# Kernel optimization log

Hardware: AMD Instinct MI355X
Metric: run time of the kernel (lower is better)

## Reference

```python
import jax, jax.numpy as jnp
import numpy as np

DIM = 1024
H = 16
D = DIM // H  # 64
EPS = 1e-6


def _rmsnorm(x, scale):
    # per-last-dim RMSNorm, computed in fp32 like the torch code
    rms = jax.lax.rsqrt(jnp.mean(x * x, axis=-1, keepdims=True) + EPS)
    return x * rms * scale


def _apply_rope(xq, xk, pe):
    # xq, xk: [B,H,L,D]; pe: [1,1,L,D/2,2,2]
    B, h, L, d = xq.shape
    xq_ = xq.reshape(B, h, L, d // 2, 1, 2)
    xk_ = xk.reshape(B, h, L, d // 2, 1, 2)
    xq_out = pe[..., 0] * xq_[..., 0] + pe[..., 1] * xq_[..., 1]  # [B,H,L,D/2,2]
    xk_out = pe[..., 0] * xk_[..., 0] + pe[..., 1] * xk_[..., 1]
    return xq_out.reshape(B, h, L, d), xk_out.reshape(B, h, L, d)


def setup_inputs() -> dict:
    key = jax.random.key(0)
    ks = jax.random.split(key, 6)
    B, L = 2, 2048
    x = jax.random.normal(ks[0], (B, L, DIM), dtype=jnp.float32)
    pe = jax.random.normal(ks[1], (1, 1, L, D // 2, 2, 2), dtype=jnp.float32)
    qkv_w = jax.random.normal(ks[2], (3 * DIM, DIM), dtype=jnp.float32) * (DIM ** -0.5)
    q_scale = jnp.ones((D,), dtype=jnp.float32)
    k_scale = jnp.ones((D,), dtype=jnp.float32)
    proj_w = jax.random.normal(ks[3], (DIM, DIM), dtype=jnp.float32) * (DIM ** -0.5)
    proj_b = jnp.zeros((DIM,), dtype=jnp.float32)
    return {"x": x, "pe": pe, "qkv_w": qkv_w, "q_scale": q_scale,
            "k_scale": k_scale, "proj_w": proj_w, "proj_b": proj_b}


def reference(x, pe, qkv_w, q_scale, k_scale, proj_w, proj_b):
    B, L, _ = x.shape
    x_c = jnp.clip(jnp.nan_to_num(x, nan=0.0, posinf=0.0, neginf=0.0), -10000.0, 10000.0)
    qkv = x_c @ qkv_w.T  # [B,L,3*DIM] (qkv_bias=False)
    qkv = jnp.nan_to_num(qkv, nan=0.0, posinf=0.0, neginf=0.0)
    # 'B L (K H D) -> K B H L D'
    qkv = qkv.reshape(B, L, 3, H, D).transpose(2, 0, 3, 1, 4)
    q, k, v = qkv[0], qkv[1], qkv[2]  # each [B,H,L,D]
    q = _rmsnorm(q, q_scale)
    k = _rmsnorm(k, k_scale)
    q, k = _apply_rope(q, k, pe)
    # scaled dot product attention (no mask)
    scores = jnp.einsum('bhqd,bhkd->bhqk', q, k) * (D ** -0.5)
    attn = jax.nn.softmax(scores, axis=-1)
    out = jnp.einsum('bhqk,bhkd->bhqd', attn, v)
    out = out.transpose(0, 2, 1, 3).reshape(B, L, H * D)  # 'B H L D -> B L (H D)'
    out = jnp.clip(out, -10000.0, 10000.0)
    return out @ proj_w.T + proj_b
```

## Files before the change

kernel.cpp:

```cpp
#include <hip/hip_runtime.h>
#include <hip/hip_bf16.h>

#define DIMC 1024
#define HEADS 16
#define HD 64
#define BATCH 2
#define SEQ 2048

typedef __bf16 bf16;
typedef __bf16 bf16x4 __attribute__((ext_vector_type(4)));
typedef __bf16 bf16x8 __attribute__((ext_vector_type(8)));
typedef float f32x4 __attribute__((ext_vector_type(4)));

typedef const __attribute__((address_space(1))) void* gas_t;
typedef __attribute__((address_space(3))) void* las_t;

__device__ inline f32x4 mfma_bf16(bf16x8 a, bf16x8 b, f32x4 c) {
    return __builtin_amdgcn_mfma_f32_16x16x32_bf16(a, b, c, 0, 0, 0);
}

__device__ inline void st8(bf16* p, bf16x8 v) {
    *(bf16x4*)p       = *(bf16x4*)&v;
    *(bf16x4*)(p + 4) = *((bf16x4*)&v + 1);
}
__device__ inline bf16x8 ld_frag(const bf16* p) {
    bf16x8 r;
    *(bf16x4*)&r       = *(const bf16x4*)p;
    *((bf16x4*)&r + 1) = *(const bf16x4*)(p + 16);
    return r;
}
__device__ inline bf16x8 ld_frag_c(const bf16* tile, int row, int kk, int lg) {
    const char* rp = (const char*)(tile + row * 64);
    const int p = row & 7;
    const int c0 = kk * 4 + (lg >> 1);
    const int ib = (lg & 1) * 8;
    bf16x8 r;
    *(bf16x4*)&r       = *(const bf16x4*)(rp + ((((c0) ^ p) << 4) | ib));
    *((bf16x4*)&r + 1) = *(const bf16x4*)(rp + ((((c0 + 2) ^ p) << 4) | ib));
    return r;
}

__device__ inline void swz_tile(int nx, int& m0, int& n0) {
    int flat = blockIdx.y * nx + blockIdx.x;
    int cpx = (nx * gridDim.y) >> 3;
    int s = (flat & 7) * cpx + (flat >> 3);
    n0 = (s % nx) * 128;
    m0 = (s / nx) * 128;
}

__global__ __launch_bounds__(256) void k_prep_all(const float* __restrict__ x,
                                                  const float* __restrict__ qw,
                                                  const float* __restrict__ pw,
                                                  bf16* __restrict__ xb,
                                                  bf16* __restrict__ wqkv,
                                                  bf16* __restrict__ wproj) {
    int idx = blockIdx.x * 1024 + threadIdx.x;
#pragma unroll
    for (int j = 0; j < 4; ++j, idx += 256) {
        if (idx < 1048576) {
            float4 v = ((const float4*)x)[idx];
            float a[4] = {v.x, v.y, v.z, v.w};
            bf16x4 o;
#pragma unroll
            for (int q = 0; q < 4; ++q) {
                float f = a[q];
                f = __builtin_isfinite(f) ? fminf(fmaxf(f, -10000.f), 10000.f) : 0.f;
                o[q] = (bf16)f;
            }
            ((bf16x4*)xb)[idx] = o;
        } else if (idx < 1835008) {
            int i2 = idx - 1048576;
            float4 v = ((const float4*)qw)[i2];
            bf16x4 o = {(bf16)v.x, (bf16)v.y, (bf16)v.z, (bf16)v.w};
            ((bf16x4*)wqkv)[i2] = o;
        } else {
            int i2 = idx - 1835008;
            float4 v = ((const float4*)pw)[i2];
            bf16x4 o = {(bf16)v.x, (bf16)v.y, (bf16)v.z, (bf16)v.w};
            ((bf16x4*)wproj)[i2] = o;
        }
    }
}

template <bool OUT_BF16, bool BIAS, bool SANITIZE>
__global__ __launch_bounds__(256) void k_gemm_bt(const bf16* __restrict__ A,
                                                 const bf16* __restrict__ Bt,
                                                 void* __restrict__ Cv,
                                                 const float* __restrict__ bias,
                                                 int N, int K) {
    __shared__ alignas(16) bf16 As[128 * 64];
    __shared__ alignas(16) bf16 Bs[128 * 64];
    const int t = threadIdx.x;
    int m0, n0;
    swz_tile(N >> 7, m0, n0);
    const int w = t >> 6, lane = t & 63;
    const int wm = (w >> 1) * 64, wn = (w & 1) * 64;
    const int lr = lane & 15, lg = lane >> 4;
    const int srow = lane >> 3;
    const int scol = ((lane & 7) ^ srow) * 8;

    f32x4 acc[4][4];
#pragma unroll
    for (int i = 0; i < 4; ++i)
#pragma unroll
        for (int j = 0; j < 4; ++j) acc[i][j] = 0.0f;

    for (int k0 = 0; k0 < K; k0 += 64) {
#pragma unroll
        for (int i = 0; i < 4; ++i) {
            int rg = w * 32 + i * 8;
            __builtin_amdgcn_global_load_lds(
                (gas_t)(A + (size_t)(m0 + rg + srow) * K + k0 + scol),
                (las_t)(As + rg * 64), 16, 0, 0);
            __builtin_amdgcn_global_load_lds(
                (gas_t)(Bt + (size_t)(n0 + rg + srow) * K + k0 + scol),
                (las_t)(Bs + rg * 64), 16, 0, 0);
        }
        __syncthreads();
#pragma unroll
        for (int kk = 0; kk < 2; ++kk) {
            bf16x8 af[4], bfr[4];
#pragma unroll
            for (int mi = 0; mi < 4; ++mi)
                af[mi] = ld_frag_c(As, wm + mi * 16 + lr, kk, lg);
#pragma unroll
            for (int ni = 0; ni < 4; ++ni)
                bfr[ni] = ld_frag_c(Bs, wn + ni * 16 + lr, kk, lg);
#pragma unroll
            for (int mi = 0; mi < 4; ++mi)
#pragma unroll
                for (int ni = 0; ni < 4; ++ni)
                    acc[mi][ni] = mfma_bf16(af[mi], bfr[ni], acc[mi][ni]);
        }
        __syncthreads();
    }
#pragma unroll
    for (int mi = 0; mi < 4; ++mi) {
#pragma unroll
        for (int ni = 0; ni < 4; ++ni) {
            int col = n0 + wn + ni * 16 + lr;
            float bval = BIAS ? bias[col] : 0.f;
#pragma unroll
            for (int r = 0; r < 4; ++r) {
                int row = m0 + wm + mi * 16 + lg * 4 + r;
                float v = acc[mi][ni][r];
                if (SANITIZE) v = __builtin_isfinite(v) ? v : 0.f;
                v += bval;
                if (OUT_BF16)
                    ((bf16*)Cv)[(size_t)row * N + col] = (bf16)v;
                else
                    ((float*)Cv)[(size_t)row * N + col] = v;
            }
        }
    }
}

__global__ __launch_bounds__(256) void k_gemm_qkv(const bf16* __restrict__ A,
                                                  const bf16* __restrict__ Bt,
                                                  const float* __restrict__ pe,
                                                  const float* __restrict__ q_scale,
                                                  const float* __restrict__ k_scale,
                                                  bf16* __restrict__ qb,
                                                  bf16* __restrict__ kb,
                                                  bf16* __restrict__ vt) {
    __shared__ alignas(16) bf16 As[128 * 64];
    __shared__ alignas(16) bf16 Bs[128 * 64];
    const int K = DIMC, t = threadIdx.x;
    int m0, n0;
    swz_tile(24, m0, n0);
    const int w = t >> 6, lane = t & 63;
    const int wm = (w >> 1) * 64, wn = (w & 1) * 64;
    const int lr = lane & 15, lg = lane >> 4;
    const int srow = lane >> 3;
    const int scol = ((lane & 7) ^ srow) * 8;

    f32x4 acc[4][4];
#pragma unroll
    for (int i = 0; i < 4; ++i)
#pragma unroll
        for (int j = 0; j < 4; ++j) acc[i][j] = 0.0f;

    for (int k0 = 0; k0 < K; k0 += 64) {
#pragma unroll
        for (int i = 0; i < 4; ++i) {
            int rg = w * 32 + i * 8;
            __builtin_amdgcn_global_load_lds(
                (gas_t)(A + (size_t)(m0 + rg + srow) * K + k0 + scol),
                (las_t)(As + rg * 64), 16, 0, 0);
            __builtin_amdgcn_global_load_lds(
                (gas_t)(Bt + (size_t)(n0 + rg + srow) * K + k0 + scol),
                (las_t)(Bs + rg * 64), 16, 0, 0);
        }
        __syncthreads();
#pragma unroll
        for (int kk = 0; kk < 2; ++kk) {
            bf16x8 af[4], bfr[4];
#pragma unroll
            for (int mi = 0; mi < 4; ++mi)
                af[mi] = ld_frag_c(As, wm + mi * 16 + lr, kk, lg);
#pragma unroll
            for (int ni = 0; ni < 4; ++ni)
                bfr[ni] = ld_frag_c(Bs, wn + ni * 16 + lr, kk, lg);
#pragma unroll
            for (int mi = 0; mi < 4; ++mi)
#pragma unroll
                for (int ni = 0; ni < 4; ++ni)
                    acc[mi][ni] = mfma_bf16(af[mi], bfr[ni], acc[mi][ni]);
        }
        __syncthreads();
    }

    const int g = (n0 + wn) >> 6;
    const int sel = g >> 4;
    const int hh = g & 15;
    const int row0 = m0 + wm;
    const int bb = row0 >> 11;
    const int l0 = row0 & (SEQ - 1);
    const size_t bhh = (size_t)(bb * HEADS + hh);

#pragma unroll
    for (int mi = 0; mi < 4; ++mi)
#pragma unroll
        for (int ni = 0; ni < 4; ++ni)
#pragma unroll
            for (int r = 0; r < 4; ++r) {
                float v = acc[mi][ni][r];
                acc[mi][ni][r] = __builtin_isfinite(v) ? v : 0.f;
            }

    if (sel == 2) {
#pragma unroll
        for (int mi = 0; mi < 4; ++mi)
#pragma unroll
            for (int ni = 0; ni < 4; ++ni) {
                bf16x4 ov;
#pragma unroll
                for (int r = 0; r < 4; ++r) ov[r] = (bf16)acc[mi][ni][r];
                *(bf16x4*)(vt + (bhh * HD + ni * 16 + lr) * SEQ +
                           l0 + mi * 16 + lg * 4) = ov;
            }
    } else {
        const float* sc = sel ? k_scale : q_scale;
        bf16* dst = sel ? kb : qb;
        const float oscale = sel ? 1.0f : 0.125f * 1.44269504088896340736f;
        float scv[4];
#pragma unroll
        for (int ni = 0; ni < 4; ++ni) scv[ni] = sc[ni * 16 + lr];
#pragma unroll
        for (int mi = 0; mi < 4; ++mi) {
#pragma unroll
            for (int r = 0; r < 4; ++r) {
                float ss = 0.f;
#pragma unroll
                for (int ni = 0; ni < 4; ++ni)
                    ss += acc[mi][ni][r] * acc[mi][ni][r];
                ss += __shfl_xor(ss, 1, 64);
                ss += __shfl_xor(ss, 2, 64);
                ss += __shfl_xor(ss, 4, 64);
                ss += __shfl_xor(ss, 8, 64);
                float rms = rsqrtf(ss * (1.f / 64.f) + 1e-6f);
                int l = l0 + mi * 16 + lg * 4 + r;
                const float* peb = pe + (size_t)l * 128 + (lr & 1) * 2;
                bf16* db = dst + (bhh * SEQ + l) * HD + lr;
#pragma unroll
                for (int ni = 0; ni < 4; ++ni) {
                    float e = acc[mi][ni][r] * rms * scv[ni];
                    float p = __shfl_xor(e, 1, 64);
                    float2 pv = *(const float2*)(peb + (ni * 8 + (lr >> 1)) * 4);
                    float ee = (lr & 1) ? p : e;
                    float eo = (lr & 1) ? e : p;
                    db[ni * 16] = (bf16)((pv.x * ee + pv.y * eo) * oscale);
                }
            }
        }
    }
}

__global__ __launch_bounds__(512) void k_attn(const bf16* __restrict__ Q,
                                              const bf16* __restrict__ Kb,
                                              const bf16* __restrict__ Vt,
                                              bf16* __restrict__ O) {
    __shared__ bf16 Ks[2][128][68];
    __shared__ bf16 Vs[2][2][64][68];
    const int bid = blockIdx.x;
    const int s_id = (bid & 7) * 64 + (bid >> 3);
    const int qt = s_id & 15, bh = s_id >> 4;
    const int b = bh >> 4, h = bh & 15;
    const int t = threadIdx.x, w = t >> 6, lane = t & 63;
    const int lr = lane & 15, lg = lane >> 4;
    const size_t baseQK = (size_t)bh * SEQ * HD;
    const size_t baseVt = (size_t)bh * HD * SEQ;

    const bf16* qp = Q + baseQK + (size_t)(qt * 128 + w * 16 + lr) * HD;
    bf16x8 qf0 = ld_frag(qp + lg * 4);
    bf16x8 qf1 = ld_frag(qp + 32 + lg * 4);

    const int sr = t >> 3, sc8 = (t & 7) * 8;
    const bf16* kg0 = Kb + baseQK + (size_t)sr * HD + sc8;
    const bf16* vg0 = Vt + baseVt + (size_t)sr * SEQ + sc8;
    {
        bf16x8 k0 = *(const bf16x8*)(kg0);
        bf16x8 k1 = *(const bf16x8*)(kg0 + (size_t)64 * HD);
        bf16x8 v0 = *(const bf16x8*)(vg0);
        bf16x8 v1 = *(const bf16x8*)(vg0 + 64);
        st8(&Ks[0][sr][sc8], k0);
        st8(&Ks[0][64 + sr][sc8], k1);
        st8(&Vs[0][0][sr][sc8], v0);
        st8(&Vs[0][1][sr][sc8], v1);
    }
    __syncthreads();

    bf16x8 ones;
#pragma unroll
    for (int j = 0; j < 8; ++j) ones[j] = (bf16)1.0f;

    f32x4 oacc[4];
#pragma unroll
    for (int i = 0; i < 4; ++i) oacc[i] = 0.0f;
    f32x4 lacc = 0.0f;

    int cur = 0;
    for (int kt = 0; kt < SEQ / 128; ++kt) {
        bf16x8 k0r, k1r, v0r, v1r;
        const bool pf = (kt + 1) < SEQ / 128;
        if (pf) {
            const bf16* kg = kg0 + (size_t)(kt + 1) * 128 * HD;
            const bf16* vg = vg0 + (kt + 1) * 128;
            k0r = *(const bf16x8*)(kg);
            k1r = *(const bf16x8*)(kg + (size_t)64 * HD);
            v0r = *(const bf16x8*)(vg);
            v1r = *(const bf16x8*)(vg + 64);
        }
        __builtin_amdgcn_s_setprio(1);
        f32x4 s[8];
#pragma unroll
        for (int nk = 0; nk < 8; ++nk) {
            f32x4 a = 0.0f;
            a = mfma_bf16(ld_frag(&Ks[cur][nk * 16 + lr][lg * 4]), qf0, a);
            a = mfma_bf16(ld_frag(&Ks[cur][nk * 16 + lr][32 + lg * 4]), qf1, a);
            s[nk] = a;
        }
        __builtin_amdgcn_s_setprio(0);
        bf16x8 pa[4];
#pragma unroll
        for (int c = 0; c < 4; ++c)
#pragma unroll
            for (int j = 0; j < 4; ++j) {
                pa[c][j]     = (bf16)exp2f(s[2 * c][j]);
                pa[c][4 + j] = (bf16)exp2f(s[2 * c + 1][j]);
            }
        __builtin_amdgcn_s_setprio(1);
#pragma unroll
        for (int c = 0; c < 4; ++c) lacc = mfma_bf16(ones, pa[c], lacc);
#pragma unroll
        for (int nd = 0; nd < 4; ++nd)
#pragma unroll
            for (int c = 0; c < 4; ++c)
                oacc[nd] = mfma_bf16(
                    ld_frag(&Vs[cur][c >> 1][nd * 16 + lr][(c & 1) * 32 + lg * 4]),
                    pa[c], oacc[nd]);
        __builtin_amdgcn_s_setprio(0);
        if (pf) {
            st8(&Ks[cur ^ 1][sr][sc8], k0r);
            st8(&Ks[cur ^ 1][64 + sr][sc8], k1r);
            st8(&Vs[cur ^ 1][0][sr][sc8], v0r);
            st8(&Vs[cur ^ 1][1][sr][sc8], v1r);
        }
        __syncthreads();
        cur ^= 1;
    }
    {
        float inv = 1.f / lacc[0];
        int q = qt * 128 + w * 16 + lr;
#pragma unroll
        for (int nd = 0; nd < 4; ++nd) {
            bf16x4 ov;
#pragma unroll
            for (int r2 = 0; r2 < 4; ++r2) {
                float v = oacc[nd][r2] * inv;
                v = fminf(fmaxf(v, -10000.f), 10000.f);
                ov[r2] = (bf16)v;
            }
            *(bf16x4*)(O + ((size_t)(b * SEQ + q)) * DIMC + h * HD + nd * 16 + lg * 4) = ov;
        }
    }
}

extern "C" void kernel_launch(void* const* d_in, const int* in_sizes, int n_in,
                              void* d_out, int out_size, void* d_ws, size_t ws_size,
                              hipStream_t stream) {
    const float* x = (const float*)d_in[0];
    const float* pe = (const float*)d_in[1];
    const float* qkv_w = (const float*)d_in[2];
    const float* q_scale = (const float*)d_in[3];
    const float* k_scale = (const float*)d_in[4];
    const float* proj_w = (const float*)d_in[5];
    const float* proj_b = (const float*)d_in[6];
    float* out = (float*)d_out;
    char* ws = (char*)d_ws;

    bf16* xb = (bf16*)(ws);
    bf16* wqkv = (bf16*)(ws + (8u << 20));
    bf16* wproj = (bf16*)(ws + (14u << 20));
    bf16* ao = (bf16*)(ws + (16u << 20));
    bf16* qb = (bf16*)(ws + (24u << 20));
    bf16* kb = (bf16*)(ws + (32u << 20));
    bf16* vt = (bf16*)(ws + (40u << 20));

    k_prep_all<<<2048, 256, 0, stream>>>(x, qkv_w, proj_w, xb, wqkv, wproj);
    k_gemm_qkv<<<dim3(24, 32), 256, 0, stream>>>(xb, wqkv, pe, q_scale, k_scale,
                                                 qb, kb, vt);
    k_attn<<<512, 512, 0, stream>>>(qb, kb, vt, ao);
    k_gemm_bt<false, true, false>
        <<<dim3(8, 32), 256, 0, stream>>>(ao, wproj, (void*)out, proj_b, 1024, 1024);
}
```

Baseline: 148.3 us.

## Permute K layout of GEMM operands so MFMA fragments load as single 16-byte reads

The prep kernel now writes x, qkv weights and proj weights in a K-permuted order, and the attention output is stored in the same permuted column order. The GEMM fragment loads then become one contiguous 16-byte swizzled LDS read instead of two 8-byte reads. Because both operands share the same K permutation, the dot products are unchanged. The goal is fewer LDS instructions in the GEMM inner loops, paid for with scattered global reads in prep and a more complex layout contract across kernels.

```diff
diff --git a/kernel.cpp b/kernel.cpp
--- a/kernel.cpp
+++ b/kernel.cpp
@@ -29,15 +29,14 @@
     *((bf16x4*)&r + 1) = *(const bf16x4*)(p + 16);
     return r;
 }
-__device__ inline bf16x8 ld_frag_c(const bf16* tile, int row, int kk, int lg) {
-    const char* rp = (const char*)(tile + row * 64);
-    const int p = row & 7;
-    const int c0 = kk * 4 + (lg >> 1);
-    const int ib = (lg & 1) * 8;
-    bf16x8 r;
-    *(bf16x4*)&r       = *(const bf16x4*)(rp + ((((c0) ^ p) << 4) | ib));
-    *((bf16x4*)&r + 1) = *(const bf16x4*)(rp + ((((c0 + 2) ^ p) << 4) | ib));
-    return r;
+__device__ inline bf16x8 ld_frag8(const bf16* tile, int row, int s) {
+    return *(const bf16x8*)(tile + row * 64 + (((s) ^ (row & 7)) << 3));
+}
+__device__ inline int perm_src4(int d4) {
+    int G = d4 & 15;
+    int s = G >> 1, h = G & 1;
+    int srcG = ((s >> 2) << 3) + (h << 2) + (s & 3);
+    return (d4 & ~15) | srcG;
 }
 
 __device__ inline void swz_tile(int nx, int& m0, int& n0) {
@@ -58,7 +57,7 @@
 #pragma unroll
     for (int j = 0; j < 4; ++j, idx += 256) {
         if (idx < 1048576) {
-            float4 v = ((const float4*)x)[idx];
+            float4 v = ((const float4*)x)[perm_src4(idx)];
             float a[4] = {v.x, v.y, v.z, v.w};
             bf16x4 o;
 #pragma unroll
@@ -70,12 +69,12 @@
             ((bf16x4*)xb)[idx] = o;
         } else if (idx < 1835008) {
             int i2 = idx - 1048576;
-            float4 v = ((const float4*)qw)[i2];
+            float4 v = ((const float4*)qw)[perm_src4(i2)];
             bf16x4 o = {(bf16)v.x, (bf16)v.y, (bf16)v.z, (bf16)v.w};
             ((bf16x4*)wqkv)[i2] = o;
         } else {
             int i2 = idx - 1835008;
-            float4 v = ((const float4*)pw)[i2];
+            float4 v = ((const float4*)pw)[perm_src4(i2)];
             bf16x4 o = {(bf16)v.x, (bf16)v.y, (bf16)v.z, (bf16)v.w};
             ((bf16x4*)wproj)[i2] = o;
         }
@@ -122,10 +121,10 @@
             bf16x8 af[4], bfr[4];
 #pragma unroll
             for (int mi = 0; mi < 4; ++mi)
-                af[mi] = ld_frag_c(As, wm + mi * 16 + lr, kk, lg);
+                af[mi] = ld_frag8(As, wm + mi * 16 + lr, kk * 4 + lg);
 #pragma unroll
             for (int ni = 0; ni < 4; ++ni)
-                bfr[ni] = ld_frag_c(Bs, wn + ni * 16 + lr, kk, lg);
+                bfr[ni] = ld_frag8(Bs, wn + ni * 16 + lr, kk * 4 + lg);
 #pragma unroll
             for (int mi = 0; mi < 4; ++mi)
 #pragma unroll
@@ -194,18 +193,18 @@
         __syncthreads();
 #pragma unroll
         for (int kk = 0; kk < 2; ++kk) {
-            bf16x8 af[4], bfr[4];
+            bf16x8 xf[4], wf[4];
+#pragma unroll
+            for (int i = 0; i < 4; ++i)
+                xf[i] = ld_frag8(As, wm + i * 16 + lr, kk * 4 + lg);
+#pragma unroll
+            for (int i = 0; i < 4; ++i)
+                wf[i] = ld_frag8(Bs, wn + i * 16 + lr, kk * 4 + lg);
 #pragma unroll
             for (int mi = 0; mi < 4; ++mi)
-                af[mi] = ld_frag_c(As, wm + mi * 16 + lr, kk, lg);
-#pragma unroll
-            for (int ni = 0; ni < 4; ++ni)
-                bfr[ni] = ld_frag_c(Bs, wn + ni * 16 + lr, kk, lg);
-#pragma unroll
-            for (int mi = 0; mi < 4; ++mi)
 #pragma unroll
                 for (int ni = 0; ni < 4; ++ni)
-                    acc[mi][ni] = mfma_bf16(af[mi], bfr[ni], acc[mi][ni]);
+                    acc[mi][ni] = mfma_bf16(xf[mi], wf[ni], acc[mi][ni]);
         }
         __syncthreads();
     }
@@ -381,7 +380,8 @@
                 v = fminf(fmaxf(v, -10000.f), 10000.f);
                 ov[r2] = (bf16)v;
             }
-            *(bf16x4*)(O + ((size_t)(b * SEQ + q)) * DIMC + h * HD + nd * 16 + lg * 4) = ov;
+            int colb = (((nd >> 1) * 4 + lg) << 3) + (nd & 1) * 4;
+            *(bf16x4*)(O + ((size_t)(b * SEQ + q)) * DIMC + h * HD + colb) = ov;
         }
     }
 }
```

New measurement: 137.3 us (median of 2 runs). 7.4% less time.
